# Kernel tuning notes

Hardware: AMD Instinct MI355X
Metric: run time of the kernel (lower is better)

## Reference

```python
import jax, jax.numpy as jnp
import numpy as np

PATCH, STRIDE, NUM_PROJ, NBINS = 7, 1, 16, 2 ** 16
B, C, H, W = 2, 3, 384, 384


def gaussian_kernel(size=7, sigma=1.2):
    x = jnp.arange(size, dtype=jnp.float32)
    # faithful to original: exp(...)**2 (square applied OUTSIDE the exp)
    return jnp.exp((x - size // 2) ** 2 / (-2.0 * sigma ** 2)) ** 2


def extract_patches(img, p, s):
    # Equivalent of F.unfold: [b, c, h, w] -> [b, N, c*p*p], torch channel-major feature order
    b, c, h, w = img.shape
    Ho = (h - p) // s + 1
    Wo = (w - p) // s + 1
    cols = [img[:, :, i:i + (Ho - 1) * s + 1:s, j:j + (Wo - 1) * s + 1:s]
            for i in range(p) for j in range(p)]
    pat = jnp.stack(cols, axis=2)  # [b, c, p*p, Ho, Wo]
    return pat.reshape(b, c * p * p, Ho * Wo).transpose(0, 2, 1)  # [b, N, c*p*p]


def hist_distance(px, py):
    # px, py: [N] projected values for one (batch, projection) pair
    min_v = jnp.minimum(py.min(), px.min())
    max_v = jnp.maximum(py.max(), px.max())
    scale = max_v - min_v
    # scatter-set 1s into a 65536-bin histogram at data-dependent indices
    y_idx = jnp.floor((NBINS - 1) * (py - min_v) / scale).astype(jnp.int32)
    y_hist = jnp.zeros((NBINS,), jnp.float32).at[y_idx].set(1.0)
    # valid conv1d with 7-tap gaussian (symmetric kernel, so corr == conv)
    y_hist = jnp.convolve(y_hist, gaussian_kernel(), mode='valid')  # [NBINS-6]
    y_hist = jnp.minimum(y_hist, 1.0)
    Wd = y_hist.shape[0]
    # grid_sample (bilinear, align_corners=False, zero padding) on a 1-tall image == 1D linear interp
    gx = 2.0 * (px - min_v) / scale - 1.0
    ix = ((gx + 1.0) * Wd - 1.0) / 2.0
    x0 = jnp.floor(ix)
    w1 = ix - x0
    x0i = x0.astype(jnp.int32)
    x1i = x0i + 1
    v0 = jnp.where((x0i >= 0) & (x0i < Wd), y_hist[jnp.clip(x0i, 0, Wd - 1)], 0.0)
    v1 = jnp.where((x1i >= 0) & (x1i < Wd), y_hist[jnp.clip(x1i, 0, Wd - 1)], 0.0)
    return -(v0 * (1.0 - w1) + v1 * w1).sum()


def setup_inputs() -> dict:
    key = jax.random.key(0)
    k1, k2, k3 = jax.random.split(key, 3)
    x = jax.random.normal(k1, (B, C, H, W), dtype=jnp.float32)
    y = jax.random.normal(k2, (B, C, H, W), dtype=jnp.float32)
    rand = jax.random.normal(k3, (B, C * PATCH * PATCH, NUM_PROJ), dtype=jnp.float32)
    return {"x": x, "y": y, "rand": rand}


def reference(x, y, rand):
    xp = extract_patches(x, PATCH, STRIDE)  # [b, N, d]
    yp = extract_patches(y, PATCH, STRIDE)
    # torch.std(dim=0) is unbiased (ddof=1)
    r = rand / jnp.std(rand, axis=1, keepdims=True, ddof=1)  # [b, d, P]
    proj_x = jnp.einsum('bnd,bdp->bpn', xp, r)
    proj_y = jnp.einsum('bnd,bdp->bpn', yp, r)
    losses = jax.vmap(jax.vmap(hist_distance))(proj_x, proj_y)  # [b, P]
    per_image = losses.sum(axis=1) / NUM_PROJ
    return per_image.mean()  # batch_reduction='mean'
```

## Files before the change

kernel.cpp:

```cpp
#include <hip/hip_runtime.h>
#include <math.h>
#include <stdint.h>

#define NPROJ 16
#define NBINS 65536
#define WD (NBINS - 6)
#define HB 65792
#define BMW 2056
#define B_ 2
#define C_ 3
#define H_ 384
#define W_ 384
#define HO 378
#define NPAT (HO * HO)
#define DF 147
#define BP 32
#define TSTR 24

__device__ inline unsigned f2key(float f) {
    unsigned u = __float_as_uint(f);
    return (u & 0x80000000u) ? ~u : (u | 0x80000000u);
}
__device__ inline float key2f(unsigned k) {
    unsigned u = (k & 0x80000000u) ? (k ^ 0x80000000u) : ~k;
    return __uint_as_float(u);
}

__global__ __launch_bounds__(64) void k_rnorm(const float* __restrict__ rnd,
                                              float* __restrict__ rnorm,
                                              unsigned* __restrict__ keys,
                                              float* __restrict__ out) {
    int bp = blockIdx.x;
    int b = bp / NPROJ, p = bp % NPROJ;
    int lane = threadIdx.x;
    if (lane == 0) {
        keys[2 * bp] = 0xFFFFFFFFu;
        keys[2 * bp + 1] = 0u;
        if (bp == 0) out[0] = 0.f;
    }
    float s = 0.f, s2 = 0.f;
    for (int d = lane; d < DF; d += 64) {
        float v = rnd[((size_t)b * DF + d) * NPROJ + p];
        s += v; s2 += v * v;
    }
    for (int o = 32; o > 0; o >>= 1) { s += __shfl_down(s, o); s2 += __shfl_down(s2, o); }
    s = __shfl(s, 0); s2 = __shfl(s2, 0);
    float mean = s / (float)DF;
    float var = (s2 - (float)DF * mean * mean) / (float)(DF - 1);
    float inv = 1.0f / sqrtf(var);
    for (int d = lane; d < DF; d += 64) {
        size_t idx = ((size_t)b * DF + d) * NPROJ + p;
        rnorm[idx] = rnd[idx] * inv;
    }
}

#define T1H 32
#define T1W 16
__global__ __launch_bounds__(256) void k_projmm(const float* __restrict__ ximg,
                                                const float* __restrict__ yimg,
                                                const float* __restrict__ rnorm,
                                                float* __restrict__ px,
                                                float* __restrict__ py,
                                                unsigned* __restrict__ keys) {
    __shared__ float tile[C_][T1H + 6][TSTR];
    __shared__ float red_mn[4][NPROJ], red_mx[4][NPROJ];
    int bz = blockIdx.z;
    int b = bz >> 1, isy = bz & 1;
    const float* img = isy ? yimg : ximg;
    float* proj = isy ? py : px;
    int tid = threadIdx.x;
    int tx = tid & 15, ty = tid >> 4;
    int h0 = blockIdx.y * T1H, w0 = blockIdx.x * T1W;

    for (int c = 0; c < C_; c++)
        for (int i = tid; i < (T1H + 6) * (T1W + 6); i += 256) {
            int r = i / (T1W + 6), col = i % (T1W + 6);
            int h = h0 + r, w = w0 + col;
            tile[c][r][col] = (h < H_ && w < W_)
                ? img[((size_t)(b * C_ + c) * H_ + h) * W_ + w] : 0.f;
        }
    __syncthreads();

    const float* wbase = rnorm + (size_t)b * DF * NPROJ;

    float acc[2][NPROJ];
#pragma unroll
    for (int q = 0; q < 2; q++)
#pragma unroll
        for (int p = 0; p < NPROJ; p++) acc[q][p] = 0.f;

    for (int c = 0; c < C_; c++)
        for (int i = 0; i < 7; i++)
#pragma unroll
            for (int j = 0; j < 7; j++) {
                const float* wrow = wbase + (c * 49 + i * 7 + j) * NPROJ;
                float wv[NPROJ];
#pragma unroll
                for (int p = 0; p < NPROJ; p++) wv[p] = wrow[p];
                float pix0 = tile[c][ty + i][tx + j];
                float pix1 = tile[c][ty + 16 + i][tx + j];
#pragma unroll
                for (int p = 0; p < NPROJ; p++) {
                    acc[0][p] = fmaf(pix0, wv[p], acc[0][p]);
                    acc[1][p] = fmaf(pix1, wv[p], acc[1][p]);
                }
            }

    int wo = w0 + tx;
    int ho0 = h0 + ty, ho1 = h0 + ty + 16;
    bool vm0 = (ho0 < HO) && (wo < HO);
    bool vm1 = (ho1 < HO) && (wo < HO);

    if (vm0) {
        size_t n = (size_t)ho0 * HO + wo;
#pragma unroll
        for (int p = 0; p < NPROJ; p++)
            proj[((size_t)(b * NPROJ + p)) * NPAT + n] = acc[0][p];
    }
    if (vm1) {
        size_t n = (size_t)ho1 * HO + wo;
#pragma unroll
        for (int p = 0; p < NPROJ; p++)
            proj[((size_t)(b * NPROJ + p)) * NPAT + n] = acc[1][p];
    }

    float pmn[NPROJ], pmx[NPROJ];
#pragma unroll
    for (int p = 0; p < NPROJ; p++) {
        float mn = INFINITY, mx = -INFINITY;
        if (vm0) { mn = acc[0][p]; mx = acc[0][p]; }
        if (vm1) { mn = fminf(mn, acc[1][p]); mx = fmaxf(mx, acc[1][p]); }
        pmn[p] = mn; pmx[p] = mx;
    }
#pragma unroll
    for (int o = 1; o < 64; o <<= 1) {
#pragma unroll
        for (int p = 0; p < NPROJ; p++) {
            pmn[p] = fminf(pmn[p], __shfl_xor(pmn[p], o));
            pmx[p] = fmaxf(pmx[p], __shfl_xor(pmx[p], o));
        }
    }
    int wv4 = tid >> 6;
    if ((tid & 63) == 0) {
#pragma unroll
        for (int p = 0; p < NPROJ; p++) { red_mn[wv4][p] = pmn[p]; red_mx[wv4][p] = pmx[p]; }
    }
    __syncthreads();
    if (tid < NPROJ) {
        float mn = fminf(fminf(red_mn[0][tid], red_mn[1][tid]),
                         fminf(red_mn[2][tid], red_mn[3][tid]));
        float mx = fmaxf(fmaxf(red_mx[0][tid], red_mx[1][tid]),
                         fmaxf(red_mx[2][tid], red_mx[3][tid]));
        atomicMin(&keys[2 * (b * NPROJ + tid)], f2key(mn));
        atomicMax(&keys[2 * (b * NPROJ + tid) + 1], f2key(mx));
    }
}

__global__ __launch_bounds__(256) void k_scatter(const float* __restrict__ py,
                                                 const unsigned* __restrict__ keys,
                                                 uint8_t* __restrict__ hist8) {
    int bp = blockIdx.y;
    float mn = key2f(keys[2 * bp]);
    float sc = key2f(keys[2 * bp + 1]) - mn;
    const float4* src = (const float4*)(py + (size_t)bp * NPAT);
    uint8_t* h = hist8 + (size_t)bp * HB + 8;
    const int n4 = NPAT / 4;
    for (int i = blockIdx.x * blockDim.x + threadIdx.x; i < n4;
         i += gridDim.x * blockDim.x) {
        float4 v = src[i];
        int i0 = (int)floorf(65535.f * (v.x - mn) / sc);
        int i1 = (int)floorf(65535.f * (v.y - mn) / sc);
        int i2 = (int)floorf(65535.f * (v.z - mn) / sc);
        int i3 = (int)floorf(65535.f * (v.w - mn) / sc);
        h[min(max(i0, 0), 65535)] = 1;
        h[min(max(i1, 0), 65535)] = 1;
        h[min(max(i2, 0), 65535)] = 1;
        h[min(max(i3, 0), 65535)] = 1;
    }
}

__global__ __launch_bounds__(256) void k_compress(const uint8_t* __restrict__ hist8,
                                                  uint32_t* __restrict__ bitmap) {
    int bp = blockIdx.y;
    const uint8_t* src = hist8 + (size_t)bp * HB;
    uint32_t* dst = bitmap + (size_t)bp * BMW;
    for (int d = blockIdx.x * blockDim.x + threadIdx.x; d < BMW;
         d += gridDim.x * blockDim.x) {
        const uint4* s = (const uint4*)(src + 32 * d);
        uint4 a = s[0], b = s[1];
        uint32_t u[8] = { a.x, a.y, a.z, a.w, b.x, b.y, b.z, b.w };
        uint32_t w = 0;
#pragma unroll
        for (int k = 0; k < 8; k++) {
            uint32_t nib = (u[k] | (u[k] >> 7) | (u[k] >> 14) | (u[k] >> 21)) & 0xFu;
            w |= nib << (4 * k);
        }
        dst[d] = w;
    }
}

__global__ __launch_bounds__(256) void k_gather(const float* __restrict__ px,
                                                const unsigned* __restrict__ keys,
                                                const uint32_t* __restrict__ bitmap,
                                                float* __restrict__ out) {
    __shared__ float2 lut[256];
    __shared__ float sred[4];
    int bp = blockIdx.y;
    int tid = threadIdx.x;

    float g[7];
#pragma unroll
    for (int k = 0; k < 7; k++) {
        float d = (float)(k - 3);
        g[k] = expf(-(d * d) / 1.44f);
    }
    {
        int m = tid;
        float f[8];
#pragma unroll
        for (int k = 0; k < 8; k++) f[k] = (float)((m >> k) & 1);
        float s0 = g[0] * f[0] + g[1] * f[1] + g[2] * f[2] + g[3] * f[3]
                 + g[4] * f[4] + g[5] * f[5] + g[6] * f[6];
        float s1 = g[0] * f[1] + g[1] * f[2] + g[2] * f[3] + g[3] * f[4]
                 + g[4] * f[5] + g[5] * f[6] + g[6] * f[7];
        lut[m] = make_float2(fminf(s0, 1.f), fminf(s1, 1.f));
    }
    __syncthreads();

    float mn = key2f(keys[2 * bp]);
    float sc = key2f(keys[2 * bp + 1]) - mn;
    const float4* src = (const float4*)(px + (size_t)bp * NPAT);
    const uint8_t* bm = (const uint8_t*)(bitmap + (size_t)bp * BMW);

    float acc = 0.f;
    const int n4 = NPAT / 4;
    for (int i = blockIdx.x * blockDim.x + threadIdx.x; i < n4;
         i += gridDim.x * blockDim.x) {
        float4 v4 = src[i];
        float vv[4] = { v4.x, v4.y, v4.z, v4.w };
#pragma unroll
        for (int j = 0; j < 4; j++) {
            float v = vv[j];
            float t = (v - mn) / sc;
            float ix = t * (float)WD - 0.5f;
            float x0 = floorf(ix);
            float w1 = ix - x0;
            int x0i = (int)x0;
            int bit0 = 8 + x0i;
            uint32_t u;
            __builtin_memcpy(&u, bm + 2 * (bit0 >> 4), 4);
            uint32_t w8 = (u >> (bit0 & 15)) & 0xFFu;
            float2 sv = lut[w8];
            float r0 = (x0i >= 0) ? sv.x : 0.f;
            float r1 = (x0i + 1 < WD) ? sv.y : 0.f;
            acc += r0 * (1.f - w1) + r1 * w1;
        }
    }
    for (int o = 32; o > 0; o >>= 1) acc += __shfl_down(acc, o);
    int wv4 = tid >> 6;
    if ((tid & 63) == 0) sred[wv4] = acc;
    __syncthreads();
    if (tid == 0) {
        float t = sred[0] + sred[1] + sred[2] + sred[3];
        atomicAdd(out, -t * (1.0f / 32.0f));
    }
}

extern "C" void kernel_launch(void* const* d_in, const int* in_sizes, int n_in,
                              void* d_out, int out_size, void* d_ws, size_t ws_size,
                              hipStream_t stream) {
    (void)in_sizes; (void)n_in; (void)out_size; (void)ws_size;
    const float* x = (const float*)d_in[0];
    const float* y = (const float*)d_in[1];
    const float* rnd = (const float*)d_in[2];
    float* out = (float*)d_out;

    float* ws = (float*)d_ws;
    float* rnorm = ws;
    float* px = rnorm + (size_t)B_ * DF * NPROJ;
    float* py = px + (size_t)BP * NPAT;
    unsigned* keys = (unsigned*)(py + (size_t)BP * NPAT);
    uint8_t* hist8 = (uint8_t*)(keys + 2 * BP);
    uint32_t* bitmap = (uint32_t*)(hist8 + (size_t)BP * HB);

    k_rnorm<<<BP, 64, 0, stream>>>(rnd, rnorm, keys, out);
    hipMemsetAsync(hist8, 0, (size_t)BP * HB, stream);

    dim3 g1(384 / T1W, 384 / T1H, 2 * B_);
    k_projmm<<<g1, 256, 0, stream>>>(x, y, rnorm, px, py, keys);

    k_scatter<<<dim3(70, BP), 256, 0, stream>>>(py, keys, hist8);
    k_compress<<<dim3(9, BP), 256, 0, stream>>>(hist8, bitmap);
    k_gather<<<dim3(70, BP), 256, 0, stream>>>(px, keys, bitmap, out);
}
```

Before: 121.0 us.

## Build histogram bitmap in LDS with atomics, drop byte histogram and compress pass

The scatter kernel now sets bits in a per-block shared-memory bitmap with atomicOr and merges it into the global bitmap, so the 2MB byte histogram, its memset and the compress kernel go away. The gather kernel copies the bitmap into LDS and reads bits from there, and the projection kernel stages the normalized weights in LDS and reads them as float4. The scatter grid shrinks to 8 blocks per projection, which cuts parallelism while each block does more LDS atomics.

```diff
diff --git a/kernel.cpp b/kernel.cpp
--- a/kernel.cpp
+++ b/kernel.cpp
@@ -5,7 +5,6 @@
 #define NPROJ 16
 #define NBINS 65536
 #define WD (NBINS - 6)
-#define HB 65792
 #define BMW 2056
 #define B_ 2
 #define C_ 3
@@ -62,6 +61,7 @@
                                                 float* __restrict__ px,
                                                 float* __restrict__ py,
                                                 unsigned* __restrict__ keys) {
+    __shared__ float wlds[DF][NPROJ];
     __shared__ float tile[C_][T1H + 6][TSTR];
     __shared__ float red_mn[4][NPROJ], red_mx[4][NPROJ];
     int bz = blockIdx.z;
@@ -72,6 +72,8 @@
     int tx = tid & 15, ty = tid >> 4;
     int h0 = blockIdx.y * T1H, w0 = blockIdx.x * T1W;
 
+    for (int i = tid; i < DF * NPROJ; i += 256)
+        ((float*)wlds)[i] = rnorm[(size_t)b * DF * NPROJ + i];
     for (int c = 0; c < C_; c++)
         for (int i = tid; i < (T1H + 6) * (T1W + 6); i += 256) {
             int r = i / (T1W + 6), col = i % (T1W + 6);
@@ -81,8 +83,6 @@
         }
     __syncthreads();
 
-    const float* wbase = rnorm + (size_t)b * DF * NPROJ;
-
     float acc[2][NPROJ];
 #pragma unroll
     for (int q = 0; q < 2; q++)
@@ -93,10 +93,12 @@
         for (int i = 0; i < 7; i++)
 #pragma unroll
             for (int j = 0; j < 7; j++) {
-                const float* wrow = wbase + (c * 49 + i * 7 + j) * NPROJ;
-                float wv[NPROJ];
-#pragma unroll
-                for (int p = 0; p < NPROJ; p++) wv[p] = wrow[p];
+                const float4* wp4 = (const float4*)&wlds[c * 49 + i * 7 + j][0];
+                float4 w0v = wp4[0], w1v = wp4[1], w2v = wp4[2], w3v = wp4[3];
+                float wv[NPROJ] = { w0v.x, w0v.y, w0v.z, w0v.w,
+                                    w1v.x, w1v.y, w1v.z, w1v.w,
+                                    w2v.x, w2v.y, w2v.z, w2v.w,
+                                    w3v.x, w3v.y, w3v.z, w3v.w };
                 float pix0 = tile[c][ty + i][tx + j];
                 float pix1 = tile[c][ty + 16 + i][tx + j];
 #pragma unroll
@@ -158,55 +160,48 @@
 
 __global__ __launch_bounds__(256) void k_scatter(const float* __restrict__ py,
                                                  const unsigned* __restrict__ keys,
-                                                 uint8_t* __restrict__ hist8) {
+                                                 unsigned* __restrict__ bitmap) {
+    __shared__ unsigned lbm[BMW];
     int bp = blockIdx.y;
+    int tid = threadIdx.x;
+    for (int i = tid; i < BMW; i += 256) lbm[i] = 0u;
+    __syncthreads();
+
     float mn = key2f(keys[2 * bp]);
     float sc = key2f(keys[2 * bp + 1]) - mn;
     const float4* src = (const float4*)(py + (size_t)bp * NPAT);
-    uint8_t* h = hist8 + (size_t)bp * HB + 8;
     const int n4 = NPAT / 4;
-    for (int i = blockIdx.x * blockDim.x + threadIdx.x; i < n4;
+    for (int i = blockIdx.x * blockDim.x + tid; i < n4;
          i += gridDim.x * blockDim.x) {
         float4 v = src[i];
-        int i0 = (int)floorf(65535.f * (v.x - mn) / sc);
-        int i1 = (int)floorf(65535.f * (v.y - mn) / sc);
-        int i2 = (int)floorf(65535.f * (v.z - mn) / sc);
-        int i3 = (int)floorf(65535.f * (v.w - mn) / sc);
-        h[min(max(i0, 0), 65535)] = 1;
-        h[min(max(i1, 0), 65535)] = 1;
-        h[min(max(i2, 0), 65535)] = 1;
-        h[min(max(i3, 0), 65535)] = 1;
-    }
-}
-
-__global__ __launch_bounds__(256) void k_compress(const uint8_t* __restrict__ hist8,
-                                                  uint32_t* __restrict__ bitmap) {
-    int bp = blockIdx.y;
-    const uint8_t* src = hist8 + (size_t)bp * HB;
-    uint32_t* dst = bitmap + (size_t)bp * BMW;
-    for (int d = blockIdx.x * blockDim.x + threadIdx.x; d < BMW;
-         d += gridDim.x * blockDim.x) {
-        const uint4* s = (const uint4*)(src + 32 * d);
-        uint4 a = s[0], b = s[1];
-        uint32_t u[8] = { a.x, a.y, a.z, a.w, b.x, b.y, b.z, b.w };
-        uint32_t w = 0;
-#pragma unroll
-        for (int k = 0; k < 8; k++) {
-            uint32_t nib = (u[k] | (u[k] >> 7) | (u[k] >> 14) | (u[k] >> 21)) & 0xFu;
-            w |= nib << (4 * k);
-        }
-        dst[d] = w;
+        float vv[4] = { v.x, v.y, v.z, v.w };
+#pragma unroll
+        for (int j = 0; j < 4; j++) {
+            int idx = (int)floorf(65535.f * (vv[j] - mn) / sc);
+            int bit = 8 + min(max(idx, 0), 65535);
+            atomicOr(&lbm[bit >> 5], 1u << (bit & 31));
+        }
+    }
+    __syncthreads();
+    unsigned* dst = bitmap + (size_t)bp * BMW;
+    for (int i = tid; i < BMW; i += 256) {
+        unsigned w = lbm[i];
+        if (w) atomicOr(&dst[i], w);
     }
 }
 
 __global__ __launch_bounds__(256) void k_gather(const float* __restrict__ px,
                                                 const unsigned* __restrict__ keys,
-                                                const uint32_t* __restrict__ bitmap,
+                                                const unsigned* __restrict__ bitmap,
                                                 float* __restrict__ out) {
+    __shared__ unsigned lbm[BMW];
     __shared__ float2 lut[256];
     __shared__ float sred[4];
     int bp = blockIdx.y;
     int tid = threadIdx.x;
+
+    const unsigned* gbm = bitmap + (size_t)bp * BMW;
+    for (int i = tid; i < BMW; i += 256) lbm[i] = gbm[i];
 
     float g[7];
 #pragma unroll
@@ -230,11 +225,10 @@
     float mn = key2f(keys[2 * bp]);
     float sc = key2f(keys[2 * bp + 1]) - mn;
     const float4* src = (const float4*)(px + (size_t)bp * NPAT);
-    const uint8_t* bm = (const uint8_t*)(bitmap + (size_t)bp * BMW);
 
     float acc = 0.f;
     const int n4 = NPAT / 4;
-    for (int i = blockIdx.x * blockDim.x + threadIdx.x; i < n4;
+    for (int i = blockIdx.x * blockDim.x + tid; i < n4;
          i += gridDim.x * blockDim.x) {
         float4 v4 = src[i];
         float vv[4] = { v4.x, v4.y, v4.z, v4.w };
@@ -247,9 +241,9 @@
             float w1 = ix - x0;
             int x0i = (int)x0;
             int bit0 = 8 + x0i;
-            uint32_t u;
-            __builtin_memcpy(&u, bm + 2 * (bit0 >> 4), 4);
-            uint32_t w8 = (u >> (bit0 & 15)) & 0xFFu;
+            int w = bit0 >> 5, s = bit0 & 31;
+            uint64_t d = (uint64_t)lbm[w] | ((uint64_t)lbm[w + 1] << 32);
+            uint32_t w8 = (uint32_t)(d >> s) & 0xFFu;
             float2 sv = lut[w8];
             float r0 = (x0i >= 0) ? sv.x : 0.f;
             float r1 = (x0i + 1 < WD) ? sv.y : 0.f;
@@ -280,16 +274,14 @@
     float* px = rnorm + (size_t)B_ * DF * NPROJ;
     float* py = px + (size_t)BP * NPAT;
     unsigned* keys = (unsigned*)(py + (size_t)BP * NPAT);
-    uint8_t* hist8 = (uint8_t*)(keys + 2 * BP);
-    uint32_t* bitmap = (uint32_t*)(hist8 + (size_t)BP * HB);
+    unsigned* bitmap = keys + 2 * BP;
 
     k_rnorm<<<BP, 64, 0, stream>>>(rnd, rnorm, keys, out);
-    hipMemsetAsync(hist8, 0, (size_t)BP * HB, stream);
+    hipMemsetAsync(bitmap, 0, (size_t)BP * BMW * sizeof(unsigned), stream);
 
     dim3 g1(384 / T1W, 384 / T1H, 2 * B_);
     k_projmm<<<g1, 256, 0, stream>>>(x, y, rnorm, px, py, keys);
 
-    k_scatter<<<dim3(70, BP), 256, 0, stream>>>(py, keys, hist8);
-    k_compress<<<dim3(9, BP), 256, 0, stream>>>(hist8, bitmap);
+    k_scatter<<<dim3(8, BP), 256, 0, stream>>>(py, keys, bitmap);
     k_gather<<<dim3(70, BP), 256, 0, stream>>>(px, keys, bitmap, out);
 }
```

Result: faster. 118.0 us (-2.5%).
